# Performance work log

Hardware: AMD Instinct MI355X
Metric: run time of the kernel (lower is better)

## Reference

```python
import jax, jax.numpy as jnp
import numpy as np

WH, WW = 8, 8            # window height/width
N = WH * WW              # tokens per window
C = 128                  # in_channels
HEADS = 8
SCALE = HEADS ** -0.5    # note: module scales by num_heads**-0.5, not head_dim**-0.5


def _rel_index():
    # Faithful port of get_relative_position_index (torch.meshgrid default = 'ij')
    coords = np.stack(np.meshgrid(np.arange(WH), np.arange(WW), indexing='ij'))
    flat = coords.reshape(2, -1)
    rel = (flat[:, :, None] - flat[:, None, :]).transpose(1, 2, 0)
    rel[:, :, 0] += WH - 1
    rel[:, :, 1] += WW - 1
    rel[:, :, 0] *= 2 * WW - 1
    return jnp.asarray(rel.sum(-1), dtype=jnp.int32)  # (N, N)


def setup_inputs() -> dict:
    key = jax.random.key(0)
    ks = jax.random.split(key, 8)
    B, H, W = 4, 256, 256
    p = lambda k, shape: jax.random.normal(k, shape, jnp.float32) * 0.02
    return {
        'x': jax.random.normal(ks[0], (B, C, H, W), jnp.float32),
        'ln1_g': jnp.ones((C,), jnp.float32), 'ln1_b': jnp.zeros((C,), jnp.float32),
        'w_qkv': p(ks[1], (C, 3 * C)), 'b_qkv': jnp.zeros((3 * C,), jnp.float32),
        'w_proj': p(ks[2], (C, C)), 'b_proj': jnp.zeros((C,), jnp.float32),
        'bias_table': p(ks[3], ((2 * WH - 1) * (2 * WW - 1), HEADS)),
        'ln2_g': jnp.ones((C,), jnp.float32), 'ln2_b': jnp.zeros((C,), jnp.float32),
        'w_fc1': p(ks[4], (C, 4 * C)), 'b_fc1': jnp.zeros((4 * C,), jnp.float32),
        'w_fc2': p(ks[5], (4 * C, C)), 'b_fc2': jnp.zeros((C,), jnp.float32),
        'rel_index': _rel_index(),
    }


def _ln(x, g, b):
    m = x.mean(-1, keepdims=True)
    v = ((x - m) ** 2).mean(-1, keepdims=True)
    return (x - m) * jax.lax.rsqrt(v + 1e-5) * g + b


def reference(x, ln1_g, ln1_b, w_qkv, b_qkv, w_proj, b_proj, bias_table,
              ln2_g, ln2_b, w_fc1, b_fc1, w_fc2, b_fc2, rel_index):
    B, Cc, H, W = x.shape
    hd = Cc // HEADS
    # window partition: (B, C, H, W) -> (B*nWin, N, C)
    win = x.reshape(B, Cc, H // WH, WH, W // WW, WW)
    win = win.transpose(0, 2, 4, 3, 5, 1).reshape(-1, N, Cc)
    # --- relative self-attention branch ---
    h = _ln(win, ln1_g, ln1_b)
    qkv = (h @ w_qkv + b_qkv).reshape(-1, N, 3, HEADS, hd)
    q, k, v = qkv[:, :, 0], qkv[:, :, 1], qkv[:, :, 2]  # (Bw, N, heads, hd)
    # gather per-pair relative position bias from the learned table
    bias = bias_table[rel_index.reshape(-1)].reshape(N, N, HEADS).transpose(2, 0, 1)  # (heads, N, N)
    logits = jnp.einsum('bqhd,bkhd->bhqk', q * SCALE, k) + bias[None]
    attn = jax.nn.softmax(logits, axis=-1)
    o = jnp.einsum('bhqk,bkhd->bqhd', attn, v).reshape(-1, N, Cc)
    win = win + (o @ w_proj + b_proj)
    # --- MLP branch ---
    h2 = _ln(win, ln2_g, ln2_b)
    win = win + (jax.nn.gelu(h2 @ w_fc1 + b_fc1, approximate=False) @ w_fc2 + b_fc2)
    # window reverse: (B*nWin, N, C) -> (B, C, H, W)
    out = win.reshape(B, H // WH, W // WW, WH, WW, Cc)
    out = out.transpose(0, 5, 1, 3, 2, 4).reshape(B, Cc, H, W)
    return out
```

## Files before the change

kernel.cpp:

```cpp
#include <hip/hip_runtime.h>
#include <hip/hip_bf16.h>
#include <stdint.h>

typedef __bf16 bf16;
typedef __bf16 bf16x8 __attribute__((ext_vector_type(8)));
typedef float  f32x4  __attribute__((ext_vector_type(4)));
typedef float  f32x16 __attribute__((ext_vector_type(16)));

#define MFMA16(a,b,c) __builtin_amdgcn_mfma_f32_16x16x32_bf16(a,b,c,0,0,0)
#define MFMA32(a,b,c) __builtin_amdgcn_mfma_f32_32x32x16_bf16(a,b,c,0,0,0)

__device__ __forceinline__ f32x4 zero4() { f32x4 z; z[0]=0.f; z[1]=0.f; z[2]=0.f; z[3]=0.f; return z; }

__device__ __forceinline__ uint32_t packbf(float lo, float hi) {
    union { bf16 b[2]; uint32_t u; } t;
    t.b[0] = (bf16)lo; t.b[1] = (bf16)hi;
    return t.u;
}
__device__ __forceinline__ bf16x8 frag_from_words(uint32_t w0, uint32_t w1, uint32_t w2, uint32_t w3) {
    union { uint32_t u[4]; bf16x8 v; } t;
    t.u[0] = w0; t.u[1] = w1; t.u[2] = w2; t.u[3] = w3;
    return t.v;
}
__device__ __forceinline__ float uf(uint32_t u) {
    union { uint32_t u; float f; } t; t.u = u; return t.f;
}
__device__ __forceinline__ float gelu_f(float u) {
    float u2 = u * u;
    float y  = u * (0.7978845608f + 0.0356774081f * u2);
    float e  = __expf(2.0f * y);
    float t  = 1.0f - 2.0f / (e + 1.0f);
    return 0.5f * u * (1.0f + t);
}

__global__ __launch_bounds__(512) void prep_kernel(
    const float* __restrict__ wqkv, const float* __restrict__ wproj,
    const float* __restrict__ wfc1, const float* __restrict__ wfc2,
    const float* __restrict__ btab, const int* __restrict__ relidx,
    bf16* __restrict__ wqkvT, bf16* __restrict__ wprojT,
    bf16* __restrict__ wfc1T, bf16* __restrict__ wfc2T,
    float* __restrict__ bN)
{
    int i = blockIdx.x * 512 + threadIdx.x;
    if (i < 49152) { int n = i >> 7, k = i & 127; wqkvT[i] = (bf16)wqkv[k*384 + n]; return; }
    i -= 49152;
    if (i < 16384) { int n = i >> 7, k = i & 127; wprojT[i] = (bf16)wproj[k*128 + n]; return; }
    i -= 16384;
    if (i < 65536) { int n = i >> 7, k = i & 127; wfc1T[i] = (bf16)wfc1[k*512 + n]; return; }
    i -= 65536;
    if (i < 65536) { int n = i >> 9, k = i & 511; wfc2T[i] = (bf16)wfc2[k*128 + n]; return; }
    i -= 65536;
    if (i < 32768) { int h = i >> 12, q = (i >> 6) & 63, k = i & 63;
                     bN[i] = btab[relidx[q*64 + k]*8 + h]; }
}

__global__ __launch_bounds__(512, 4) void swin_attn(
    const float* __restrict__ x,
    const float* __restrict__ ln1_g, const float* __restrict__ ln1_b,
    const float* __restrict__ b_qkv, const float* __restrict__ b_proj,
    const bf16* __restrict__ wqkvT, const bf16* __restrict__ wprojT,
    const float* __restrict__ bN,
    float* __restrict__ win2tm)
{
    __shared__ __align__(16) char sm[49152];

    const int tid  = threadIdx.x;
    const int lane = tid & 63;
    const int wv   = tid >> 6;
    const int l15  = lane & 15;
    const int l4   = (lane >> 4) & 3;
    const int l31  = lane & 31;
    const int hi   = lane >> 5;
    const int fmt  = wv >> 1;
    const int fn0  = (wv & 1) * 64;

    const int wid = ((blockIdx.x & 7) << 9) | (blockIdx.x >> 3);
    const int bb  = wid >> 10;
    const int hw  = (wid >> 5) & 31;
    const int wwi = wid & 31;
    const size_t base = (size_t)bb * 8388608 + (size_t)hw * 2048 + (size_t)wwi * 8;
    const float* xw = x + base;

#pragma unroll
    for (int it = 0; it < 4; ++it) {
        int idx = it*512 + tid;
        int c = idx >> 4, t2 = idx & 15;
        int row = t2 >> 1, col0 = (t2 & 1) * 4;
        f32x4 v = *(const f32x4*)(xw + (size_t)c*65536 + row*256 + col0);
#pragma unroll
        for (int e = 0; e < 4; ++e) {
            int t = row*8 + col0 + e;
            *(bf16*)(sm + t*256 + ((2*c) ^ ((t&7)<<4))) = (bf16)v[e];
        }
    }
    __syncthreads();

    uint32_t winp[2][4];
#pragma unroll
    for (int r = 0; r < 4; ++r) {
        int tok = fmt*16 + l4*4 + r;
        int swz = (tok & 7) << 4;
        const char* rowp = sm + tok*256;
        uint32_t c0 = *(const uint16_t*)(rowp + ((2*(fn0 +  0 + l15)) ^ swz));
        uint32_t c1 = *(const uint16_t*)(rowp + ((2*(fn0 + 16 + l15)) ^ swz));
        uint32_t c2 = *(const uint16_t*)(rowp + ((2*(fn0 + 32 + l15)) ^ swz));
        uint32_t c3 = *(const uint16_t*)(rowp + ((2*(fn0 + 48 + l15)) ^ swz));
        winp[0][r] = c0 | (c1 << 16);
        winp[1][r] = c2 | (c3 << 16);
    }

    {
        const int t = tid >> 3, p = tid & 7;
        const int swz = (t & 7) << 4;
        float vv[16];
        float s = 0.f, s2 = 0.f;
#pragma unroll
        for (int hlf = 0; hlf < 2; ++hlf) {
            bf16x8 xv = *(const bf16x8*)(sm + t*256 + ((p*32 + hlf*16) ^ swz));
#pragma unroll
            for (int e = 0; e < 8; ++e) { float f = (float)xv[e]; vv[hlf*8+e] = f; s += f; s2 += f*f; }
        }
#pragma unroll
        for (int m = 1; m < 8; m <<= 1) { s += __shfl_xor(s, m, 64); s2 += __shfl_xor(s2, m, 64); }
        const float mean = s * 0.0078125f;
        const float rs = rsqrtf(s2 * 0.0078125f - mean*mean + 1e-5f);
#pragma unroll
        for (int hlf = 0; hlf < 2; ++hlf) {
            bf16x8 hv;
#pragma unroll
            for (int e = 0; e < 8; ++e) {
                int c = p*16 + hlf*8 + e;
                hv[e] = (bf16)((vv[hlf*8+e] - mean) * rs * ln1_g[c] + ln1_b[c]);
            }
            *(bf16x8*)(sm + 16384 + t*256 + ((p*32 + hlf*16) ^ swz)) = hv;
        }
    }
    __syncthreads();

    {
        const float SCALE = 0.35355339059327373f;
        const int nq0 = wv * 32;
        const int nv  = 256 + wv*16 + l15;
        const float bb0 = b_qkv[nq0 + l15];
        const float bb1 = b_qkv[nq0 + 16 + l15];
        const float bbv = b_qkv[nv];
        const bool isq = (nq0 < 128);
        char* rb = isq ? (sm + 16384) : (sm + 32768);
        const float sc = isq ? SCALE : 1.0f;
        const int c0 = (nq0 & 127) + l15;
        const int c1 = ((nq0 + 16) & 127) + l15;
#pragma unroll
        for (int half = 0; half < 2; ++half) {
            f32x4 a0[2], a1[2], avh[2];
#pragma unroll
            for (int m2 = 0; m2 < 2; ++m2) { a0[m2] = zero4(); a1[m2] = zero4(); avh[m2] = zero4(); }
#pragma unroll
            for (int ks = 0; ks < 4; ++ks) {
                bf16x8 bq0 = *(const bf16x8*)(wqkvT + (nq0      + l15)*128 + ks*32 + l4*8);
                bf16x8 bq1 = *(const bf16x8*)(wqkvT + (nq0 + 16 + l15)*128 + ks*32 + l4*8);
                bf16x8 bv  = *(const bf16x8*)(wqkvT + nv*128 + ks*32 + l4*8);
#pragma unroll
                for (int m2 = 0; m2 < 2; ++m2) {
                    int tok = half*32 + m2*16 + l15;
                    bf16x8 afr = *(const bf16x8*)(sm + 16384 + tok*256 + ((ks*64 + l4*16) ^ ((tok&7)<<4)));
                    a0[m2]  = MFMA16(afr, bq0, a0[m2]);
                    a1[m2]  = MFMA16(afr, bq1, a1[m2]);
                    avh[m2] = MFMA16(afr, bv,  avh[m2]);
                }
            }
            __syncthreads();
#pragma unroll
            for (int m2 = 0; m2 < 2; ++m2)
#pragma unroll
                for (int r = 0; r < 4; ++r) {
                    int tok = half*32 + m2*16 + l4*4 + r;
                    int swz = (tok & 7) << 4;
                    *(bf16*)(rb + tok*256 + ((2*c0) ^ swz)) = (bf16)((a0[m2][r] + bb0) * sc);
                    *(bf16*)(rb + tok*256 + ((2*c1) ^ swz)) = (bf16)((a1[m2][r] + bb1) * sc);
                }
            {
                int d = l15;
                char* vb = sm + wv*2048 + d*128;
                int sz = (d & 7) << 4;
#pragma unroll
                for (int m2 = 0; m2 < 2; ++m2) {
                    int t0 = half*32 + m2*16 + l4*4;
                    *(uint32_t*)(vb + ((2*t0)     ^ sz)) = packbf(avh[m2][0]+bbv, avh[m2][1]+bbv);
                    *(uint32_t*)(vb + ((2*t0 + 4) ^ sz)) = packbf(avh[m2][2]+bbv, avh[m2][3]+bbv);
                }
            }
        }
    }
    __syncthreads();

    {
        bf16x8 kf[2];
#pragma unroll
        for (int tk = 0; tk < 2; ++tk) {
            int tok = tk*32 + l31;
            kf[tk] = *(const bf16x8*)(sm + 32768 + tok*256 + ((wv*32 + hi*16) ^ ((tok&7)<<4)));
        }
        __syncthreads();
#pragma unroll
        for (int tq = 0; tq < 2; ++tq) {
            int q = tq*32 + l31;
            bf16x8 qf = *(const bf16x8*)(sm + 16384 + q*256 + ((wv*32 + hi*16) ^ ((q&7)<<4)));
            const float* bq = bN + wv*4096 + q*64 + 4*hi;
            float ss, ri;
            uint32_t own[16];
            {
                f32x16 s0, s1;
#pragma unroll
                for (int g4 = 0; g4 < 4; ++g4) {
                    f32x4 b0 = *(const f32x4*)(bq + g4*8);
                    f32x4 b1 = *(const f32x4*)(bq + 32 + g4*8);
#pragma unroll
                    for (int e = 0; e < 4; ++e) { s0[g4*4+e] = b0[e]; s1[g4*4+e] = b1[e]; }
                }
                s0 = MFMA32(kf[0], qf, s0);
                s1 = MFMA32(kf[1], qf, s1);
                ss = 0.f;
#pragma unroll
                for (int r = 0; r < 16; ++r) {
                    s0[r] = __expf(s0[r]);
                    s1[r] = __expf(s1[r]);
                    ss += s0[r] + s1[r];
                }
#pragma unroll
                for (int ks = 0; ks < 4; ++ks)
#pragma unroll
                    for (int i = 0; i < 4; ++i) {
                        const int j = 2*(i&1) + 4*((2*ks + (i>>1)) & 3) + 16*(ks>>1);
                        if (j < 16) own[ks*4+i] = packbf(s0[j], s0[j+1]);
                        else        own[ks*4+i] = packbf(s1[j-16], s1[j-15]);
                    }
            }
            ss += __shfl_xor(ss, 32, 64);
            ri = 1.0f / ss;
            f32x16 Ot;
#pragma unroll
            for (int i = 0; i < 16; ++i) Ot[i] = 0.f;
#pragma unroll
            for (int ks = 0; ks < 4; ++ks) {
                uint32_t sw0 = __shfl_xor(own[ks*4+0], 32, 64);
                uint32_t sw1 = __shfl_xor(own[ks*4+1], 32, 64);
                uint32_t sw2 = __shfl_xor(own[ks*4+2], 32, 64);
                uint32_t sw3 = __shfl_xor(own[ks*4+3], 32, 64);
                uint32_t w0 = hi ? sw2          : own[ks*4+0];
                uint32_t w1 = hi ? sw3          : own[ks*4+1];
                uint32_t w2 = hi ? own[ks*4+2]  : sw0;
                uint32_t w3 = hi ? own[ks*4+3]  : sw1;
                bf16x8 pf = frag_from_words(w0, w1, w2, w3);
                int dd = l31 & 15;
                bf16x8 vf = *(const bf16x8*)(sm + wv*2048 + dd*128
                                             + ((ks*32 + hi*16) ^ ((dd&7)<<4)));
                Ot = MFMA32(vf, pf, Ot);
            }
#pragma unroll
            for (int r = 0; r < 8; r += 2) {
                int d = (r&3) + 8*(r>>2) + 4*hi;
                *(uint32_t*)(sm + 32768 + q*256 + ((2*(wv*16 + d)) ^ ((q&7)<<4)))
                    = packbf(Ot[r]*ri, Ot[r+1]*ri);
            }
        }
    }
    __syncthreads();

    {
        f32x4 acc[4];
#pragma unroll
        for (int nt = 0; nt < 4; ++nt) acc[nt] = zero4();
#pragma unroll
        for (int ks = 0; ks < 4; ++ks) {
            int tok = fmt*16 + l15;
            bf16x8 afr = *(const bf16x8*)(sm + 32768 + tok*256 + ((ks*64 + l4*16) ^ ((tok&7)<<4)));
#pragma unroll
            for (int nt = 0; nt < 4; ++nt) {
                int n = fn0 + nt*16 + l15;
                bf16x8 bfr = *(const bf16x8*)(wprojT + n*128 + ks*32 + l4*8);
                acc[nt] = MFMA16(afr, bfr, acc[nt]);
            }
        }
        float* w2 = win2tm + (size_t)wid*8192;
#pragma unroll
        for (int nt = 0; nt < 4; ++nt) {
            int c = fn0 + nt*16 + l15;
            float bp = b_proj[c];
#pragma unroll
            for (int r = 0; r < 4; ++r) {
                int tok = fmt*16 + l4*4 + r;
                uint32_t w = winp[nt >> 1][r];
                float xr = uf((nt & 1) ? (w & 0xffff0000u) : (w << 16));
                w2[tok*128 + c] = xr + acc[nt][r] + bp;
            }
        }
    }
}

__global__ __launch_bounds__(512, 4) void swin_mlp(
    const float* __restrict__ win2tm,
    const float* __restrict__ ln2_g, const float* __restrict__ ln2_b,
    const float* __restrict__ b_fc1, const float* __restrict__ b_fc2,
    const bf16* __restrict__ wfc1T, const bf16* __restrict__ wfc2T,
    float* __restrict__ out)
{
    __shared__ __align__(16) char sm[49152];

    const int tid  = threadIdx.x;
    const int lane = tid & 63;
    const int wv   = tid >> 6;
    const int l15  = lane & 15;
    const int l4   = (lane >> 4) & 3;
    const int cw   = wv * 16 + l15;

    const int wid = ((blockIdx.x & 7) << 9) | (blockIdx.x >> 3);
    const int bb  = wid >> 10;
    const int hw  = (wid >> 5) & 31;
    const int wwi = wid & 31;
    const size_t obase = (size_t)bb * 8388608 + (size_t)hw * 2048 + (size_t)wwi * 8;
    float* outw = out + obase;
    const float* w2 = win2tm + (size_t)wid*8192;

    {
        const int t = tid >> 3, p = tid & 7;
        const int swz = (t & 7) << 4;
        float vv[16];
        float s = 0.f, s2 = 0.f;
#pragma unroll
        for (int i4 = 0; i4 < 4; ++i4) {
            f32x4 v = *(const f32x4*)(w2 + t*128 + p*16 + i4*4);
#pragma unroll
            for (int e = 0; e < 4; ++e) { float f = v[e]; vv[i4*4+e] = f; s += f; s2 += f*f; }
        }
#pragma unroll
        for (int m = 1; m < 8; m <<= 1) { s += __shfl_xor(s, m, 64); s2 += __shfl_xor(s2, m, 64); }
        const float mean = s * 0.0078125f;
        const float rs = rsqrtf(s2 * 0.0078125f - mean*mean + 1e-5f);
#pragma unroll
        for (int hlf = 0; hlf < 2; ++hlf) {
            bf16x8 hv;
#pragma unroll
            for (int e = 0; e < 8; ++e) {
                int c = p*16 + hlf*8 + e;
                hv[e] = (bf16)((vv[hlf*8+e] - mean) * rs * ln2_g[c] + ln2_b[c]);
            }
            *(bf16x8*)(sm + t*256 + ((p*32 + hlf*16) ^ swz)) = hv;
        }
    }
    __syncthreads();

    f32x4 acc2[4];
#pragma unroll
    for (int mt = 0; mt < 4; ++mt) acc2[mt] = zero4();

#define FC1_CHUNK(C4, GB)                                                          \
    {                                                                              \
        f32x4 a1[4];                                                               \
        a1[0] = zero4(); a1[1] = zero4(); a1[2] = zero4(); a1[3] = zero4();        \
        _Pragma("unroll")                                                          \
        for (int ks = 0; ks < 4; ++ks) {                                           \
            bf16x8 bfr = *(const bf16x8*)(wfc1T + ((C4)*128 + cw)*128 + ks*32 + l4*8); \
            _Pragma("unroll")                                                      \
            for (int mt = 0; mt < 4; ++mt) {                                       \
                int tok = mt*16 + l15;                                             \
                bf16x8 afr = *(const bf16x8*)(sm + tok*256 + ((ks*64 + l4*16) ^ ((tok&7)<<4))); \
                a1[mt] = MFMA16(afr, bfr, a1[mt]);                                 \
            }                                                                      \
        }                                                                          \
        float b1 = b_fc1[(C4)*128 + cw];                                           \
        _Pragma("unroll")                                                          \
        for (int mt = 0; mt < 4; ++mt)                                             \
            _Pragma("unroll")                                                      \
            for (int r = 0; r < 4; ++r) {                                          \
                int tok = mt*16 + l4*4 + r;                                        \
                float u = a1[mt][r] + b1;                                          \
                *(bf16*)((GB) + tok*256 + ((2*cw) ^ ((tok&7)<<4))) = (bf16)gelu_f(u); \
            }                                                                      \
    }

    FC1_CHUNK(0, sm + 16384)
#pragma unroll
    for (int c4 = 0; c4 < 4; ++c4) {
        __syncthreads();
        if (c4 < 3) {
            char* gb = sm + 16384 + (((c4+1)&1) << 14);
            FC1_CHUNK(c4+1, gb)
        }
        const char* gcur = sm + 16384 + ((c4&1) << 14);
#pragma unroll
        for (int ks = 0; ks < 4; ++ks) {
            bf16x8 bfr = *(const bf16x8*)(wfc2T + cw*512 + c4*128 + ks*32 + l4*8);
#pragma unroll
            for (int mt = 0; mt < 4; ++mt) {
                int tok = mt*16 + l15;
                bf16x8 afr = *(const bf16x8*)(gcur + tok*256 + ((ks*64 + l4*16) ^ ((tok&7)<<4)));
                acc2[mt] = MFMA16(afr, bfr, acc2[mt]);
            }
        }
    }
#undef FC1_CHUNK

    {
        float bf_ = b_fc2[cw];
#pragma unroll
        for (int mt = 0; mt < 4; ++mt)
#pragma unroll
            for (int r = 0; r < 4; ++r) {
                int tok = mt*16 + l4*4 + r;
                float res = w2[tok*128 + cw];
                *(float*)(sm + tok*512 + ((cw*4) ^ ((tok&15)<<4))) = res + acc2[mt][r] + bf_;
            }
    }
    __syncthreads();
#pragma unroll
    for (int it = 0; it < 4; ++it) {
        int idx = it*512 + tid;
        int c = idx >> 4, t2 = idx & 15;
        int row = t2 >> 1, col0 = (t2 & 1) * 4;
        f32x4 v;
#pragma unroll
        for (int e = 0; e < 4; ++e) {
            int t = row*8 + col0 + e;
            v[e] = *(const float*)(sm + t*512 + ((c*4) ^ ((t&15)<<4)));
        }
        *(f32x4*)(outw + (size_t)c*65536 + row*256 + col0) = v;
    }
}

__global__ __launch_bounds__(512, 4) void swin_fused(
    const float* __restrict__ x,
    const float* __restrict__ ln1_g, const float* __restrict__ ln1_b,
    const float* __restrict__ b_qkv, const float* __restrict__ b_proj,
    const float* __restrict__ ln2_g, const float* __restrict__ ln2_b,
    const float* __restrict__ b_fc1, const float* __restrict__ b_fc2,
    const bf16* __restrict__ wqkvT, const bf16* __restrict__ wprojT,
    const bf16* __restrict__ wfc1T, const bf16* __restrict__ wfc2T,
    const float* __restrict__ bN,
    float* __restrict__ out)
{
    __shared__ __align__(16) char sm[49152];

    const int tid  = threadIdx.x;
    const int lane = tid & 63;
    const int wv   = tid >> 6;
    const int l15  = lane & 15;
    const int l4   = (lane >> 4) & 3;
    const int l31  = lane & 31;
    const int hi   = lane >> 5;
    const int fmt  = wv >> 1;
    const int fn0  = (wv & 1) * 64;

    const int wid = ((blockIdx.x & 7) << 9) | (blockIdx.x >> 3);
    const int bb  = wid >> 10;
    const int hw  = (wid >> 5) & 31;
    const int wwi = wid & 31;
    const size_t base = (size_t)bb * 8388608 + (size_t)hw * 2048 + (size_t)wwi * 8;
    const float* xw   = x   + base;
    float*       outw = out + base;

#pragma unroll
    for (int it = 0; it < 4; ++it) {
        int idx = it*512 + tid;
        int c = idx >> 4, t2 = idx & 15;
        int row = t2 >> 1, col0 = (t2 & 1) * 4;
        f32x4 v = *(const f32x4*)(xw + (size_t)c*65536 + row*256 + col0);
#pragma unroll
        for (int e = 0; e < 4; ++e) {
            int t = row*8 + col0 + e;
            *(bf16*)(sm + t*256 + ((2*c) ^ ((t&7)<<4))) = (bf16)v[e];
        }
    }
    __syncthreads();

    uint32_t winp[2][4];
#pragma unroll
    for (int r = 0; r < 4; ++r) {
        int tok = fmt*16 + l4*4 + r;
        int swz = (tok & 7) << 4;
        const char* rowp = sm + tok*256;
        uint32_t c0 = *(const uint16_t*)(rowp + ((2*(fn0 +  0 + l15)) ^ swz));
        uint32_t c1 = *(const uint16_t*)(rowp + ((2*(fn0 + 16 + l15)) ^ swz));
        uint32_t c2 = *(const uint16_t*)(rowp + ((2*(fn0 + 32 + l15)) ^ swz));
        uint32_t c3 = *(const uint16_t*)(rowp + ((2*(fn0 + 48 + l15)) ^ swz));
        winp[0][r] = c0 | (c1 << 16);
        winp[1][r] = c2 | (c3 << 16);
    }

    {
        const int t = tid >> 3, p = tid & 7;
        const int swz = (t & 7) << 4;
        float vv[16];
        float s = 0.f, s2 = 0.f;
#pragma unroll
        for (int hlf = 0; hlf < 2; ++hlf) {
            bf16x8 xv = *(const bf16x8*)(sm + t*256 + ((p*32 + hlf*16) ^ swz));
#pragma unroll
            for (int e = 0; e < 8; ++e) { float f = (float)xv[e]; vv[hlf*8+e] = f; s += f; s2 += f*f; }
        }
#pragma unroll
        for (int m = 1; m < 8; m <<= 1) { s += __shfl_xor(s, m, 64); s2 += __shfl_xor(s2, m, 64); }
        const float mean = s * 0.0078125f;
        const float rs = rsqrtf(s2 * 0.0078125f - mean*mean + 1e-5f);
#pragma unroll
        for (int hlf = 0; hlf < 2; ++hlf) {
            bf16x8 hv;
#pragma unroll
            for (int e = 0; e < 8; ++e) {
                int c = p*16 + hlf*8 + e;
                hv[e] = (bf16)((vv[hlf*8+e] - mean) * rs * ln1_g[c] + ln1_b[c]);
            }
            *(bf16x8*)(sm + 16384 + t*256 + ((p*32 + hlf*16) ^ swz)) = hv;
        }
    }
    __syncthreads();

    {
        const float SCALE = 0.35355339059327373f;
        const int nq0 = wv * 32;
        const int nv  = 256 + wv*16 + l15;
        const float bb0 = b_qkv[nq0 + l15];
        const float bb1 = b_qkv[nq0 + 16 + l15];
        const float bbv = b_qkv[nv];
        const bool isq = (nq0 < 128);
        char* rb = isq ? (sm + 16384) : (sm + 32768);
        const float sc = isq ? SCALE : 1.0f;
        const int c0 = (nq0 & 127) + l15;
        const int c1 = ((nq0 + 16) & 127) + l15;
#pragma unroll
        for (int half = 0; half < 2; ++half) {
            f32x4 a0[2], a1[2], avh[2];
#pragma unroll
            for (int m2 = 0; m2 < 2; ++m2) { a0[m2] = zero4(); a1[m2] = zero4(); avh[m2] = zero4(); }
#pragma unroll
            for (int ks = 0; ks < 4; ++ks) {
                bf16x8 bq0 = *(const bf16x8*)(wqkvT + (nq0      + l15)*128 + ks*32 + l4*8);
                bf16x8 bq1 = *(const bf16x8*)(wqkvT + (nq0 + 16 + l15)*128 + ks*32 + l4*8);
                bf16x8 bv  = *(const bf16x8*)(wqkvT + nv*128 + ks*32 + l4*8);
#pragma unroll
                for (int m2 = 0; m2 < 2; ++m2) {
                    int tok = half*32 + m2*16 + l15;
                    bf16x8 afr = *(const bf16x8*)(sm + 16384 + tok*256 + ((ks*64 + l4*16) ^ ((tok&7)<<4)));
                    a0[m2]  = MFMA16(afr, bq0, a0[m2]);
                    a1[m2]  = MFMA16(afr, bq1, a1[m2]);
                    avh[m2] = MFMA16(afr, bv,  avh[m2]);
                }
            }
            __syncthreads();
#pragma unroll
            for (int m2 = 0; m2 < 2; ++m2)
#pragma unroll
                for (int r = 0; r < 4; ++r) {
                    int tok = half*32 + m2*16 + l4*4 + r;
                    int swz = (tok & 7) << 4;
                    *(bf16*)(rb + tok*256 + ((2*c0) ^ swz)) = (bf16)((a0[m2][r] + bb0) * sc);
                    *(bf16*)(rb + tok*256 + ((2*c1) ^ swz)) = (bf16)((a1[m2][r] + bb1) * sc);
                }
            {
                int d = l15;
                char* vb = sm + wv*2048 + d*128;
                int sz = (d & 7) << 4;
#pragma unroll
                for (int m2 = 0; m2 < 2; ++m2) {
                    int t0 = half*32 + m2*16 + l4*4;
                    *(uint32_t*)(vb + ((2*t0)     ^ sz)) = packbf(avh[m2][0]+bbv, avh[m2][1]+bbv);
                    *(uint32_t*)(vb + ((2*t0 + 4) ^ sz)) = packbf(avh[m2][2]+bbv, avh[m2][3]+bbv);
                }
            }
        }
    }
    __syncthreads();

    {
        bf16x8 kf[2];
#pragma unroll
        for (int tk = 0; tk < 2; ++tk) {
            int tok = tk*32 + l31;
            kf[tk] = *(const bf16x8*)(sm + 32768 + tok*256 + ((wv*32 + hi*16) ^ ((tok&7)<<4)));
        }
        __syncthreads();
#pragma unroll
        for (int tq = 0; tq < 2; ++tq) {
            int q = tq*32 + l31;
            bf16x8 qf = *(const bf16x8*)(sm + 16384 + q*256 + ((wv*32 + hi*16) ^ ((q&7)<<4)));
            const float* bq = bN + wv*4096 + q*64 + 4*hi;
            float ss, ri;
            uint32_t own[16];
            {
                f32x16 s0, s1;
#pragma unroll
                for (int g4 = 0; g4 < 4; ++g4) {
                    f32x4 b0 = *(const f32x4*)(bq + g4*8);
                    f32x4 b1 = *(const f32x4*)(bq + 32 + g4*8);
#pragma unroll
                    for (int e = 0; e < 4; ++e) { s0[g4*4+e] = b0[e]; s1[g4*4+e] = b1[e]; }
                }
                s0 = MFMA32(kf[0], qf, s0);
                s1 = MFMA32(kf[1], qf, s1);
                ss = 0.f;
#pragma unroll
                for (int r = 0; r < 16; ++r) {
                    s0[r] = __expf(s0[r]);
                    s1[r] = __expf(s1[r]);
                    ss += s0[r] + s1[r];
                }
#pragma unroll
                for (int ks = 0; ks < 4; ++ks)
#pragma unroll
                    for (int i = 0; i < 4; ++i) {
                        const int j = 2*(i&1) + 4*((2*ks + (i>>1)) & 3) + 16*(ks>>1);
                        if (j < 16) own[ks*4+i] = packbf(s0[j], s0[j+1]);
                        else        own[ks*4+i] = packbf(s1[j-16], s1[j-15]);
                    }
            }
            ss += __shfl_xor(ss, 32, 64);
            ri = 1.0f / ss;
            f32x16 Ot;
#pragma unroll
            for (int i = 0; i < 16; ++i) Ot[i] = 0.f;
#pragma unroll
            for (int ks = 0; ks < 4; ++ks) {
                uint32_t sw0 = __shfl_xor(own[ks*4+0], 32, 64);
                uint32_t sw1 = __shfl_xor(own[ks*4+1], 32, 64);
                uint32_t sw2 = __shfl_xor(own[ks*4+2], 32, 64);
                uint32_t sw3 = __shfl_xor(own[ks*4+3], 32, 64);
                uint32_t w0 = hi ? sw2          : own[ks*4+0];
                uint32_t w1 = hi ? sw3          : own[ks*4+1];
                uint32_t w2 = hi ? own[ks*4+2]  : sw0;
                uint32_t w3 = hi ? own[ks*4+3]  : sw1;
                bf16x8 pf = frag_from_words(w0, w1, w2, w3);
                int dd = l31 & 15;
                bf16x8 vf = *(const bf16x8*)(sm + wv*2048 + dd*128
                                             + ((ks*32 + hi*16) ^ ((dd&7)<<4)));
                Ot = MFMA32(vf, pf, Ot);
            }
#pragma unroll
            for (int r = 0; r < 8; r += 2) {
                int d = (r&3) + 8*(r>>2) + 4*hi;
                *(uint32_t*)(sm + 32768 + q*256 + ((2*(wv*16 + d)) ^ ((q&7)<<4)))
                    = packbf(Ot[r]*ri, Ot[r+1]*ri);
            }
        }
    }
    __syncthreads();

    float win2[4][4];
    {
        f32x4 acc[4];
#pragma unroll
        for (int nt = 0; nt < 4; ++nt) acc[nt] = zero4();
#pragma unroll
        for (int ks = 0; ks < 4; ++ks) {
            int tok = fmt*16 + l15;
            bf16x8 afr = *(const bf16x8*)(sm + 32768 + tok*256 + ((ks*64 + l4*16) ^ ((tok&7)<<4)));
#pragma unroll
            for (int nt = 0; nt < 4; ++nt) {
                int n = fn0 + nt*16 + l15;
                bf16x8 bfr = *(const bf16x8*)(wprojT + n*128 + ks*32 + l4*8);
                acc[nt] = MFMA16(afr, bfr, acc[nt]);
            }
        }
#pragma unroll
        for (int nt = 0; nt < 4; ++nt) {
            float bp = b_proj[fn0 + nt*16 + l15];
#pragma unroll
            for (int r = 0; r < 4; ++r) {
                uint32_t w = winp[nt >> 1][r];
                float xr = uf((nt & 1) ? (w & 0xffff0000u) : (w << 16));
                win2[nt][r] = xr + acc[nt][r] + bp;
            }
        }
    }

    {
        float s[4], s2[4];
#pragma unroll
        for (int r = 0; r < 4; ++r) {
            s[r]  = win2[0][r] + win2[1][r] + win2[2][r] + win2[3][r];
            s2[r] = win2[0][r]*win2[0][r] + win2[1][r]*win2[1][r]
                  + win2[2][r]*win2[2][r] + win2[3][r]*win2[3][r];
#pragma unroll
            for (int m = 1; m < 16; m <<= 1) {
                s[r]  += __shfl_xor(s[r],  m, 64);
                s2[r] += __shfl_xor(s2[r], m, 64);
            }
        }
        float2* scr = (float2*)sm;
        if (l15 == 0) {
#pragma unroll
            for (int r = 0; r < 4; ++r) {
                int tok = fmt*16 + l4*4 + r;
                scr[tok*2 + (wv&1)] = make_float2(s[r], s2[r]);
            }
        }
        __syncthreads();
        float mean[4], rstd[4];
#pragma unroll
        for (int r = 0; r < 4; ++r) {
            int tok = fmt*16 + l4*4 + r;
            float2 p = scr[tok*2 + ((wv&1)^1)];
            float tot = s[r] + p.x, tot2 = s2[r] + p.y;
            float m = tot * 0.0078125f;
            mean[r] = m;
            rstd[r] = rsqrtf(tot2*0.0078125f - m*m + 1e-5f);
        }
#pragma unroll
        for (int nt = 0; nt < 4; ++nt) {
            int c = fn0 + nt*16 + l15;
            float gg = ln2_g[c], bb2 = ln2_b[c];
#pragma unroll
            for (int r = 0; r < 4; ++r) {
                int tok = fmt*16 + l4*4 + r;
                *(bf16*)(sm + 16384 + tok*256 + ((2*c) ^ ((tok&7)<<4)))
                    = (bf16)((win2[nt][r] - mean[r]) * rstd[r] * gg + bb2);
            }
        }
    }
    __syncthreads();

    {
        f32x4 acc2[4];
#pragma unroll
        for (int nt = 0; nt < 4; ++nt) acc2[nt] = zero4();
#pragma unroll
        for (int c4 = 0; c4 < 4; ++c4) {
            char* gbuf = (c4 & 1) ? (sm + 32768) : sm;
            {
                f32x4 a1[4];
#pragma unroll
                for (int nt = 0; nt < 4; ++nt) a1[nt] = zero4();
#pragma unroll
                for (int ks = 0; ks < 4; ++ks) {
                    int tok = fmt*16 + l15;
                    bf16x8 afr = *(const bf16x8*)(sm + 16384 + tok*256 + ((ks*64 + l4*16) ^ ((tok&7)<<4)));
#pragma unroll
                    for (int nt = 0; nt < 4; ++nt) {
                        int n = c4*128 + fn0 + nt*16 + l15;
                        bf16x8 bfr = *(const bf16x8*)(wfc1T + n*128 + ks*32 + l4*8);
                        a1[nt] = MFMA16(afr, bfr, a1[nt]);
                    }
                }
#pragma unroll
                for (int nt = 0; nt < 4; ++nt) {
                    int cl = fn0 + nt*16 + l15;
                    float b1 = b_fc1[c4*128 + cl];
#pragma unroll
                    for (int r = 0; r < 4; ++r) {
                        int tok = fmt*16 + l4*4 + r;
                        float u = a1[nt][r] + b1;
                        *(bf16*)(gbuf + tok*256 + ((2*cl) ^ ((tok&7)<<4))) = (bf16)gelu_f(u);
                    }
                }
            }
            __syncthreads();
#pragma unroll
            for (int ks = 0; ks < 4; ++ks) {
                int tok = fmt*16 + l15;
                bf16x8 afr = *(const bf16x8*)(gbuf + tok*256 + ((ks*64 + l4*16) ^ ((tok&7)<<4)));
#pragma unroll
                for (int nt = 0; nt < 4; ++nt) {
                    int n = fn0 + nt*16 + l15;
                    bf16x8 bfr = *(const bf16x8*)(wfc2T + n*512 + c4*128 + ks*32 + l4*8);
                    acc2[nt] = MFMA16(afr, bfr, acc2[nt]);
                }
            }
        }
#pragma unroll
        for (int nt = 0; nt < 4; ++nt) {
            float bf_ = b_fc2[fn0 + nt*16 + l15];
#pragma unroll
            for (int r = 0; r < 4; ++r) win2[nt][r] += acc2[nt][r] + bf_;
        }
    }
    __syncthreads();

#pragma unroll
    for (int nt = 0; nt < 4; ++nt)
#pragma unroll
        for (int r = 0; r < 4; ++r) {
            int tok = fmt*16 + l4*4 + r;
            int c   = fn0 + nt*16 + l15;
            *(float*)(sm + tok*512 + ((c*4) ^ ((tok&15)<<4))) = win2[nt][r];
        }
    __syncthreads();
#pragma unroll
    for (int it = 0; it < 4; ++it) {
        int idx = it*512 + tid;
        int c = idx >> 4, t2 = idx & 15;
        int row = t2 >> 1, col0 = (t2 & 1) * 4;
        f32x4 v;
#pragma unroll
        for (int e = 0; e < 4; ++e) {
            int t = row*8 + col0 + e;
            v[e] = *(const float*)(sm + t*512 + ((c*4) ^ ((t&15)<<4)));
        }
        *(f32x4*)(outw + (size_t)c*65536 + row*256 + col0) = v;
    }
}

extern "C" void kernel_launch(void* const* d_in, const int* in_sizes, int n_in,
                              void* d_out, int out_size, void* d_ws, size_t ws_size,
                              hipStream_t stream) {
    const float* x      = (const float*)d_in[0];
    const float* ln1_g  = (const float*)d_in[1];
    const float* ln1_b  = (const float*)d_in[2];
    const float* w_qkv  = (const float*)d_in[3];
    const float* b_qkv  = (const float*)d_in[4];
    const float* w_proj = (const float*)d_in[5];
    const float* b_proj = (const float*)d_in[6];
    const float* btab   = (const float*)d_in[7];
    const float* ln2_g  = (const float*)d_in[8];
    const float* ln2_b  = (const float*)d_in[9];
    const float* w_fc1  = (const float*)d_in[10];
    const float* b_fc1  = (const float*)d_in[11];
    const float* w_fc2  = (const float*)d_in[12];
    const float* b_fc2  = (const float*)d_in[13];
    const int*   relix  = (const int*)d_in[14];
    float* out = (float*)d_out;

    char* ws = (char*)d_ws;
    bf16*  wqkvT  = (bf16*)(ws);
    bf16*  wprojT = (bf16*)(ws + 98304);
    bf16*  wfc1T  = (bf16*)(ws + 131072);
    bf16*  wfc2T  = (bf16*)(ws + 262144);
    float* bN     = (float*)(ws + 393216);
    float* win2tm = (float*)(ws + 524288);

    prep_kernel<<<dim3(448), dim3(512), 0, stream>>>(
        w_qkv, w_proj, w_fc1, w_fc2, btab, relix,
        wqkvT, wprojT, wfc1T, wfc2T, bN);

    const size_t need = 524288ull + 134217728ull;
    if (ws_size >= need) {
        swin_attn<<<dim3(4096), dim3(512), 0, stream>>>(
            x, ln1_g, ln1_b, b_qkv, b_proj, wqkvT, wprojT, bN, win2tm);
        swin_mlp<<<dim3(4096), dim3(512), 0, stream>>>(
            win2tm, ln2_g, ln2_b, b_fc1, b_fc2, wfc1T, wfc2T, out);
    } else {
        swin_fused<<<dim3(4096), dim3(512), 0, stream>>>(
            x, ln1_g, ln1_b, b_qkv, b_proj, ln2_g, ln2_b, b_fc1, b_fc2,
            wqkvT, wprojT, wfc1T, wfc2T, bN, out);
    }
}
```

Baseline: 464.0 us.

## Stream keys per half in attention and remap proj GEMM to column-per-wave

The attention loop now processes keys in two 32-token halves. Each half computes scores, exponentiates them and accumulates P·V immediately, instead of holding both score tiles and 16 packed words at once. This lowers register pressure and removes the intra-block barrier that existed so K could be cached before being overwritten. The attention output is written to the Q region instead of the K region. The projection GEMM now assigns each wave 16 output channels across all 64 tokens, so one weight fragment is loaded per k-step and reused across four token tiles instead of reloading four global weight fragments. The residual capture layout changes to match.

```diff
diff --git a/kernel.cpp b/kernel.cpp
--- a/kernel.cpp
+++ b/kernel.cpp
@@ -71,8 +71,7 @@
     const int l4   = (lane >> 4) & 3;
     const int l31  = lane & 31;
     const int hi   = lane >> 5;
-    const int fmt  = wv >> 1;
-    const int fn0  = (wv & 1) * 64;
+    const int cw   = wv*16 + l15;
 
     const int wid = ((blockIdx.x & 7) << 9) | (blockIdx.x >> 3);
     const int bb  = wid >> 10;
@@ -95,19 +94,17 @@
     }
     __syncthreads();
 
-    uint32_t winp[2][4];
-#pragma unroll
-    for (int r = 0; r < 4; ++r) {
-        int tok = fmt*16 + l4*4 + r;
-        int swz = (tok & 7) << 4;
-        const char* rowp = sm + tok*256;
-        uint32_t c0 = *(const uint16_t*)(rowp + ((2*(fn0 +  0 + l15)) ^ swz));
-        uint32_t c1 = *(const uint16_t*)(rowp + ((2*(fn0 + 16 + l15)) ^ swz));
-        uint32_t c2 = *(const uint16_t*)(rowp + ((2*(fn0 + 32 + l15)) ^ swz));
-        uint32_t c3 = *(const uint16_t*)(rowp + ((2*(fn0 + 48 + l15)) ^ swz));
-        winp[0][r] = c0 | (c1 << 16);
-        winp[1][r] = c2 | (c3 << 16);
-    }
+    uint32_t winp[4][2];
+#pragma unroll
+    for (int mt = 0; mt < 4; ++mt)
+#pragma unroll
+        for (int rp = 0; rp < 2; ++rp) {
+            int tok0 = mt*16 + l4*4 + 2*rp;
+            int tok1 = tok0 + 1;
+            uint32_t u0 = *(const uint16_t*)(sm + tok0*256 + ((2*cw) ^ ((tok0&7)<<4)));
+            uint32_t u1 = *(const uint16_t*)(sm + tok1*256 + ((2*cw) ^ ((tok1&7)<<4)));
+            winp[mt][rp] = u0 | (u1 << 16);
+        }
 
     {
         const int t = tid >> 3, p = tid & 7;
@@ -194,72 +191,61 @@
     __syncthreads();
 
     {
-        bf16x8 kf[2];
-#pragma unroll
-        for (int tk = 0; tk < 2; ++tk) {
-            int tok = tk*32 + l31;
-            kf[tk] = *(const bf16x8*)(sm + 32768 + tok*256 + ((wv*32 + hi*16) ^ ((tok&7)<<4)));
-        }
-        __syncthreads();
 #pragma unroll
         for (int tq = 0; tq < 2; ++tq) {
             int q = tq*32 + l31;
             bf16x8 qf = *(const bf16x8*)(sm + 16384 + q*256 + ((wv*32 + hi*16) ^ ((q&7)<<4)));
-            const float* bq = bN + wv*4096 + q*64 + 4*hi;
-            float ss, ri;
-            uint32_t own[16];
-            {
-                f32x16 s0, s1;
+            f32x16 Ot;
+#pragma unroll
+            for (int i = 0; i < 16; ++i) Ot[i] = 0.f;
+            float ss = 0.f;
+#pragma unroll
+            for (int kh = 0; kh < 2; ++kh) {
+                int kt = kh*32 + l31;
+                bf16x8 kfh = *(const bf16x8*)(sm + 32768 + kt*256 + ((wv*32 + hi*16) ^ ((kt&7)<<4)));
+                const float* bq = bN + wv*4096 + q*64 + kh*32 + 4*hi;
+                f32x16 s;
 #pragma unroll
                 for (int g4 = 0; g4 < 4; ++g4) {
                     f32x4 b0 = *(const f32x4*)(bq + g4*8);
-                    f32x4 b1 = *(const f32x4*)(bq + 32 + g4*8);
-#pragma unroll
-                    for (int e = 0; e < 4; ++e) { s0[g4*4+e] = b0[e]; s1[g4*4+e] = b1[e]; }
-                }
-                s0 = MFMA32(kf[0], qf, s0);
-                s1 = MFMA32(kf[1], qf, s1);
-                ss = 0.f;
-#pragma unroll
-                for (int r = 0; r < 16; ++r) {
-                    s0[r] = __expf(s0[r]);
-                    s1[r] = __expf(s1[r]);
-                    ss += s0[r] + s1[r];
-                }
-#pragma unroll
-                for (int ks = 0; ks < 4; ++ks)
+#pragma unroll
+                    for (int e = 0; e < 4; ++e) s[g4*4+e] = b0[e];
+                }
+                s = MFMA32(kfh, qf, s);
+#pragma unroll
+                for (int r = 0; r < 16; ++r) { s[r] = __expf(s[r]); ss += s[r]; }
+                uint32_t ow[8];
+#pragma unroll
+                for (int ksl = 0; ksl < 2; ++ksl)
 #pragma unroll
                     for (int i = 0; i < 4; ++i) {
-                        const int j = 2*(i&1) + 4*((2*ks + (i>>1)) & 3) + 16*(ks>>1);
-                        if (j < 16) own[ks*4+i] = packbf(s0[j], s0[j+1]);
-                        else        own[ks*4+i] = packbf(s1[j-16], s1[j-15]);
+                        const int j = 2*(i&1) + 4*((2*ksl + (i>>1)) & 3);
+                        ow[ksl*4+i] = packbf(s[j], s[j+1]);
                     }
+#pragma unroll
+                for (int ksl = 0; ksl < 2; ++ksl) {
+                    uint32_t sw0 = __shfl_xor(ow[ksl*4+0], 32, 64);
+                    uint32_t sw1 = __shfl_xor(ow[ksl*4+1], 32, 64);
+                    uint32_t sw2 = __shfl_xor(ow[ksl*4+2], 32, 64);
+                    uint32_t sw3 = __shfl_xor(ow[ksl*4+3], 32, 64);
+                    uint32_t w0  = hi ? sw2           : ow[ksl*4+0];
+                    uint32_t w1  = hi ? sw3           : ow[ksl*4+1];
+                    uint32_t w2_ = hi ? ow[ksl*4+2]   : sw0;
+                    uint32_t w3  = hi ? ow[ksl*4+3]   : sw1;
+                    bf16x8 pf = frag_from_words(w0, w1, w2_, w3);
+                    int dd = l31 & 15;
+                    int ks = 2*kh + ksl;
+                    bf16x8 vf = *(const bf16x8*)(sm + wv*2048 + dd*128
+                                                 + ((ks*32 + hi*16) ^ ((dd&7)<<4)));
+                    Ot = MFMA32(vf, pf, Ot);
+                }
             }
             ss += __shfl_xor(ss, 32, 64);
-            ri = 1.0f / ss;
-            f32x16 Ot;
-#pragma unroll
-            for (int i = 0; i < 16; ++i) Ot[i] = 0.f;
-#pragma unroll
-            for (int ks = 0; ks < 4; ++ks) {
-                uint32_t sw0 = __shfl_xor(own[ks*4+0], 32, 64);
-                uint32_t sw1 = __shfl_xor(own[ks*4+1], 32, 64);
-                uint32_t sw2 = __shfl_xor(own[ks*4+2], 32, 64);
-                uint32_t sw3 = __shfl_xor(own[ks*4+3], 32, 64);
-                uint32_t w0 = hi ? sw2          : own[ks*4+0];
-                uint32_t w1 = hi ? sw3          : own[ks*4+1];
-                uint32_t w2 = hi ? own[ks*4+2]  : sw0;
-                uint32_t w3 = hi ? own[ks*4+3]  : sw1;
-                bf16x8 pf = frag_from_words(w0, w1, w2, w3);
-                int dd = l31 & 15;
-                bf16x8 vf = *(const bf16x8*)(sm + wv*2048 + dd*128
-                                             + ((ks*32 + hi*16) ^ ((dd&7)<<4)));
-                Ot = MFMA32(vf, pf, Ot);
-            }
+            float ri = 1.0f / ss;
 #pragma unroll
             for (int r = 0; r < 8; r += 2) {
                 int d = (r&3) + 8*(r>>2) + 4*hi;
-                *(uint32_t*)(sm + 32768 + q*256 + ((2*(wv*16 + d)) ^ ((q&7)<<4)))
+                *(uint32_t*)(sm + 16384 + q*256 + ((2*(wv*16 + d)) ^ ((q&7)<<4)))
                     = packbf(Ot[r]*ri, Ot[r+1]*ri);
             }
         }
@@ -269,31 +255,28 @@
     {
         f32x4 acc[4];
 #pragma unroll
-        for (int nt = 0; nt < 4; ++nt) acc[nt] = zero4();
+        for (int mt = 0; mt < 4; ++mt) acc[mt] = zero4();
 #pragma unroll
         for (int ks = 0; ks < 4; ++ks) {
-            int tok = fmt*16 + l15;
-            bf16x8 afr = *(const bf16x8*)(sm + 32768 + tok*256 + ((ks*64 + l4*16) ^ ((tok&7)<<4)));
-#pragma unroll
-            for (int nt = 0; nt < 4; ++nt) {
-                int n = fn0 + nt*16 + l15;
-                bf16x8 bfr = *(const bf16x8*)(wprojT + n*128 + ks*32 + l4*8);
-                acc[nt] = MFMA16(afr, bfr, acc[nt]);
+            bf16x8 bfr = *(const bf16x8*)(wprojT + cw*128 + ks*32 + l4*8);
+#pragma unroll
+            for (int mt = 0; mt < 4; ++mt) {
+                int tok = mt*16 + l15;
+                bf16x8 afr = *(const bf16x8*)(sm + 16384 + tok*256 + ((ks*64 + l4*16) ^ ((tok&7)<<4)));
+                acc[mt] = MFMA16(afr, bfr, acc[mt]);
             }
         }
         float* w2 = win2tm + (size_t)wid*8192;
-#pragma unroll
-        for (int nt = 0; nt < 4; ++nt) {
-            int c = fn0 + nt*16 + l15;
-            float bp = b_proj[c];
+        float bp = b_proj[cw];
+#pragma unroll
+        for (int mt = 0; mt < 4; ++mt)
 #pragma unroll
             for (int r = 0; r < 4; ++r) {
-                int tok = fmt*16 + l4*4 + r;
-                uint32_t w = winp[nt >> 1][r];
-                float xr = uf((nt & 1) ? (w & 0xffff0000u) : (w << 16));
-                w2[tok*128 + c] = xr + acc[nt][r] + bp;
-            }
-        }
+                int tok = mt*16 + l4*4 + r;
+                uint32_t w = winp[mt][r>>1];
+                float xr = uf((r&1) ? (w & 0xffff0000u) : (w << 16));
+                w2[tok*128 + cw] = xr + acc[mt][r] + bp;
+            }
     }
 }
 
```

Result: faster. 427.6 us (median of 2 runs) (-7.9%).
